# Optimization experiments

Measured on AMD Instinct MI355X. Metric: run time of the kernel, lower is better.

Reference implementation:

```python
import jax, jax.numpy as jnp
import numpy as np
import math

D_DT, D_STATE, D_CONV = 32, 16, 4
C, P, DM, DI = 16, 256, 512, 1024


def setup_inputs() -> dict:
    key = jax.random.key(0)
    ks = jax.random.split(key, 8)
    rn = lambda k, s, sc: jax.random.normal(k, s, jnp.float32) * sc
    # dt bias init as in the module
    u = jax.random.uniform(ks[6], (DI,), jnp.float32)
    dt_bias = jnp.clip(jnp.exp(u * (math.log(0.1) - math.log(0.001))), 0.001, None)
    inv_dt_bias = dt_bias + jnp.log(-jnp.expm1(-dt_bias))
    A_log = jnp.log(jnp.tile(jnp.arange(1, D_STATE + 1, dtype=jnp.float32)[None, :], (DI, 1)))
    return {
        "x": jax.random.normal(ks[0], (C, P, DM), jnp.float32),
        "ssm_state": jnp.zeros((C, DI, D_STATE), jnp.float32),
        "in_w": rn(ks[1], (2 * DI, DM), DM ** -0.5),
        "in_b": jnp.zeros((2 * DI,), jnp.float32),
        "conv_w": rn(ks[2], (DI, DI, D_CONV), (DI * D_CONV) ** -0.5),
        "conv_b": jnp.zeros((DI,), jnp.float32),
        "param_w": rn(ks[3], (D_DT + 2 * D_STATE, DI), DI ** -0.5),
        "param_b": jnp.zeros((D_DT + 2 * D_STATE,), jnp.float32),
        "dt_w": jax.random.uniform(ks[4], (DI, D_DT), jnp.float32, -D_DT ** -0.5, D_DT ** -0.5),
        "dt_b": inv_dt_bias,
        "out_w": rn(ks[5], (DM, DI), DI ** -0.5),
        "out_b": jnp.zeros((DM,), jnp.float32),
        "A_log": A_log,
        "D": jnp.ones((DI,), jnp.float32),
    }


def reference(x, ssm_state, in_w, in_b, conv_w, conv_b, param_w, param_b,
              dt_w, dt_b, out_w, out_b, A_log, D):
    # input projection -> x, z branches          [C,P,2*DI]
    xz = x @ in_w.T + in_b
    xi, z = jnp.split(xz, 2, axis=-1)            # each [C,P,DI]
    # 'same'-ish edge padding along patch axis, then full Conv1d (valid)
    pad = ((0, 0), (D_CONV // 2, (D_CONV + 1) // 2 - 1), (0, 0))
    xi = jnp.pad(xi, pad, mode='edge')
    xi = jnp.swapaxes(xi, -1, -2)                # [C,DI,P+D_CONV-1]
    xi = jax.lax.conv_general_dilated(xi, conv_w, (1,), 'VALID',
                                      dimension_numbers=('NCH', 'OIH', 'NCH'))
    xi = xi + conv_b[None, :, None]
    xi = jax.nn.gelu(jnp.swapaxes(xi, -1, -2))   # [C,P,DI]
    # selective params
    x_db = xi @ param_w.T + param_b              # [C,P,D_DT+2*D_STATE]
    dt, B, Cm = jnp.split(x_db, (D_DT, D_DT + D_STATE), axis=-1)
    dt = jax.nn.softplus(dt @ dt_w.T + dt_b)     # [C,P,DI]
    A = -jnp.exp(A_log)                          # [DI,D_STATE]
    dA = jnp.exp(jnp.einsum('cpd,dn->pcdn', dt, A))   # [P,C,DI,D_STATE]
    dB = jnp.einsum('cpd,cpn->pcdn', dt, B)            # [P,C,DI,D_STATE]
    z = jax.nn.gelu(z)                           # (gelu applied again inside step, as in source)
    Cm_t = jnp.swapaxes(Cm, 0, 1)                # [P,C,D_STATE]
    xi_t = jnp.swapaxes(xi, 0, 1)                # [P,C,DI]
    z_t = jnp.swapaxes(z, 0, 1)                  # [P,C,DI]

    def step(s, data):
        xt, zt, dAt, dBt, Ct = data
        s = s * dAt + xt[..., None] * dBt        # [C,DI,D_STATE]
        y = jnp.einsum('cdn,cn->cd', s, Ct) + D * xt
        return s, y * jax.nn.gelu(zt)            # double gelu: faithful to source

    ssm_state, y = jax.lax.scan(step, ssm_state, (xi_t, z_t, dA, dB, Cm_t))
    y = y @ out_w.T + out_b                      # [P,C,DM]
    return jnp.swapaxes(y, 0, 1), ssm_state
```

## Files before the change

### kernel.cpp

```cpp
#include <hip/hip_runtime.h>
#include <hip/hip_bf16.h>

typedef __hip_bfloat16 bf16;
typedef short bf16x8 __attribute__((ext_vector_type(8)));
typedef float f32x4 __attribute__((ext_vector_type(4)));

#define CC 16
#define PP 256
#define DMH 512
#define DIH 1024
#define MM (CC*PP)
#define NST 16
#define NDT 32
#define LOG2E 1.44269504088896f

__device__ __forceinline__ float b2f(bf16 v){ return __bfloat162float(v); }
__device__ __forceinline__ bf16  f2b(float v){ return __float2bfloat16(v); }
__device__ __forceinline__ float us2f(ushort u){ bf16 h; *(ushort*)&h = u; return __bfloat162float(h); }

__device__ __forceinline__ float geluf(float x){
  const float u = x*(0.7978845608028654f + 0.035677408136300125f*x*x);
  const float e = __builtin_amdgcn_exp2f(2.885390081777927f*u);
  const float t = 1.0f - 2.0f*__builtin_amdgcn_rcpf(e + 1.0f);
  return 0.5f*x*(1.0f + t);
}
__device__ __forceinline__ float softplusf(float x){
  if (x > 20.0f) return x;
  const float e = __builtin_amdgcn_exp2f(x * LOG2E);
  return 0.6931471805599453f * __builtin_amdgcn_logf(1.0f + e);
}

__device__ __forceinline__ void g2l16(const bf16* g, bf16* l){
  __builtin_amdgcn_global_load_lds(
      (const __attribute__((address_space(1))) void*)g,
      (__attribute__((address_space(3))) void*)(uint32_t)(uintptr_t)l,
      16, 0, 0);
}

__global__ void prep_all(const float* __restrict__ x, const float* __restrict__ in_w,
                         const float* __restrict__ out_w, const float* __restrict__ param_w,
                         const float* __restrict__ conv_w, const float* __restrict__ dt_w,
                         const float* __restrict__ in_b, const float* __restrict__ conv_b,
                         float* __restrict__ cb2p,
                         bf16* __restrict__ xbf, bf16* __restrict__ inwz,
                         bf16* __restrict__ outwb, bf16* __restrict__ pwb,
                         bf16* __restrict__ cwT, bf16* __restrict__ inwT,
                         bf16* __restrict__ dtwb)
{
  const int b = blockIdx.x, tid = threadIdx.x;
  if (b < 3136){
    const float* src; bf16* dst; int i;
    if (b < 2048)      { src = x;                       dst = xbf;   i = b*256 + tid; }
    else if (b < 2560) { src = in_w + (size_t)DIH*DMH;  dst = inwz;  i = (b-2048)*256 + tid; }
    else if (b < 3072) { src = out_w;                   dst = outwb; i = (b-2560)*256 + tid; }
    else               { src = param_w;                 dst = pwb;   i = (b-3072)*256 + tid; }
    float4 v = ((const float4*)src)[i];
    bf16 o[4] = {f2b(v.x), f2b(v.y), f2b(v.z), f2b(v.w)};
    *(ushort4*)&dst[(size_t)i*4] = *(const ushort4*)o;
  } else if (b < 7232){
    const size_t idx = (size_t)(b-3136)*256 + tid;
    const float4 v = *(const float4*)(conv_w + idx*4);
    cwT[idx]                     = f2b(v.x);
    cwT[(size_t)DIH*DIH   + idx] = f2b(v.y);
    cwT[(size_t)2*DIH*DIH + idx] = f2b(v.z);
    cwT[(size_t)3*DIH*DIH + idx] = f2b(v.w);
    __shared__ float ls[4];
    const int i = (int)(idx & 1023);
    float acc = (v.x + v.y + v.z + v.w) * in_b[i];
    for (int off = 32; off; off >>= 1) acc += __shfl_down(acc, off);
    if ((tid & 63) == 0) ls[tid >> 6] = acc;
    __syncthreads();
    if (tid == 0){
      const int o   = (int)(idx >> 10);
      const int sub = (b - 3136) & 3;
      float tot = ls[0] + ls[1] + ls[2] + ls[3];
      if (sub == 0) tot += conv_b[o];
      cb2p[sub*DIH + o] = tot;
    }
  } else if (b < 7360){
    __shared__ float T[64][65];
    const int b2 = b - 7232;
    const int i0 = (b2 >> 3)*64, m0 = (b2 & 7)*64;
    const int r = tid >> 2, c0 = (tid & 3)*16;
    #pragma unroll
    for (int t = 0; t < 4; t++){
      float4 v = *(const float4*)&in_w[(size_t)(i0 + r)*DMH + m0 + c0 + t*4];
      T[r][c0+t*4+0] = v.x; T[r][c0+t*4+1] = v.y;
      T[r][c0+t*4+2] = v.z; T[r][c0+t*4+3] = v.w;
    }
    __syncthreads();
    bf16 o[16];
    #pragma unroll
    for (int t = 0; t < 16; t++) o[t] = f2b(T[c0 + t][r]);
    *(ushort4*)&inwT[(size_t)(m0 + r)*DIH + i0 + c0]      = *(const ushort4*)&o[0];
    *(ushort4*)&inwT[(size_t)(m0 + r)*DIH + i0 + c0 + 4]  = *(const ushort4*)&o[4];
    *(ushort4*)&inwT[(size_t)(m0 + r)*DIH + i0 + c0 + 8]  = *(const ushort4*)&o[8];
    *(ushort4*)&inwT[(size_t)(m0 + r)*DIH + i0 + c0 + 12] = *(const ushort4*)&o[12];
  } else {
    const int idx4 = (b-7360)*256 + tid;
    const int d = idx4 >> 4, k4 = (idx4 & 15)*4;
    bf16 o[4] = {};
    if (k4 < 32){
      const float4 v = *(const float4*)&dt_w[(size_t)d*NDT + k4];
      o[0]=f2b(v.x); o[1]=f2b(v.y); o[2]=f2b(v.z); o[3]=f2b(v.w);
    }
    *(ushort4*)&dtwb[(size_t)d*64 + k4] = *(const ushort4*)o;
  }
}

#define TBK 64

template<int EPI, int NFRAG>
__launch_bounds__(256)
__global__ void mfma_gemm(const bf16* __restrict__ A, int lda,
                          const bf16* __restrict__ B, int ldb,
                          const float* __restrict__ bias,
                          float* __restrict__ outF,
                          bf16* __restrict__ outB0,
                          int ldo, int K, int azs, int ozs, int kzs)
{
  __shared__ bf16 As[128*TBK];
  __shared__ bf16 Bs[32*NFRAG*TBK];
  const int tid  = threadIdx.x;
  const int lane = tid & 63;
  const int wave = tid >> 6;
  const int wr = (wave >> 1) * 64;
  const int wc = (wave & 1) * 16 * NFRAG;
  const int mBase = blockIdx.x * 128;
  const int nBase = blockIdx.y * (32*NFRAG);
  A += (size_t)blockIdx.z * azs;
  const int nOff = blockIdx.z * ozs;
  const int koff = blockIdx.z * kzs;

  f32x4 acc[4][NFRAG] = {};

  for (int k0 = 0; k0 < K; k0 += TBK) {
    __syncthreads();
    #pragma unroll
    for (int it = 0; it < 4; it++) {
      const int idx = it*256 + tid;
      const int r = idx >> 3;
      const int cs = (idx & 7) ^ (r & 7);
      const bf16* ga = A + (size_t)(mBase + r)*lda + koff + k0 + cs*8;
      g2l16(ga, &As[(size_t)idx*8]);
    }
    #pragma unroll
    for (int it = 0; it < NFRAG; it++) {
      const int idx = it*256 + tid;
      const int r = idx >> 3;
      const int cs = (idx & 7) ^ (r & 7);
      const bf16* gb = B + (size_t)(nBase + r)*ldb + koff + k0 + cs*8;
      g2l16(gb, &Bs[(size_t)idx*8]);
    }
    __syncthreads();
    #pragma unroll
    for (int ks = 0; ks < 2; ks++) {
      bf16x8 af[4], bfr[NFRAG];
      #pragma unroll
      for (int r = 0; r < 4; r++){
        const int rr = wr + r*16 + (lane & 15);
        const int ch = (ks*4 + (lane>>4)) ^ (rr & 7);
        af[r] = *(const bf16x8*)&As[rr*TBK + ch*8];
      }
      #pragma unroll
      for (int c = 0; c < NFRAG; c++){
        const int rn = wc + c*16 + (lane & 15);
        const int ch = (ks*4 + (lane>>4)) ^ (rn & 7);
        bfr[c] = *(const bf16x8*)&Bs[rn*TBK + ch*8];
      }
      #pragma unroll
      for (int r = 0; r < 4; r++)
        #pragma unroll
        for (int c = 0; c < NFRAG; c++)
          acc[r][c] = __builtin_amdgcn_mfma_f32_16x16x32_bf16(af[r], bfr[c], acc[r][c], 0, 0, 0);
    }
  }

  const int col0 = lane & 15;
  const int row0 = (lane >> 4) * 4;
  #pragma unroll
  for (int r = 0; r < 4; r++) {
    #pragma unroll
    for (int c = 0; c < NFRAG; c++) {
      #pragma unroll
      for (int reg = 0; reg < 4; reg++) {
        const int m = mBase + wr + r*16 + row0 + reg;
        const int n = nBase + wc + c*16 + col0;
        const float av = acc[r][c][reg];
        if (EPI == 0) {
          outF[(size_t)m*ldo + n] = av + bias[n];
        } else if (EPI == 2) {
          outB0[(size_t)m*ldo + n] = f2b(geluf(geluf(av + bias[n])));
        } else if (EPI == 3) {
          outB0[(size_t)m*ldo + n + nOff] = f2b(av);
        } else if (EPI == 5) {
          const float dtv = softplusf(av + bias[n]);
          bf16 dh = f2b(dtv);
          ((ushort*)outB0)[(size_t)m*ldo + n] = *(const ushort*)&dh;
        } else if (EPI == 7) {
          const float vv = av + bias[n];
          if (n < 32) {
            bf16 dh = f2b(vv);
            ((ushort*)outB0)[(size_t)m*64 + n] = *(const ushort*)&dh;
          } else {
            ((ushort*)outB0)[(size_t)m*64 + n] = 0;
            outF[(size_t)m*32 + (n - 32)] = vv;
          }
        }
      }
    }
  }
}

__launch_bounds__(256)
__global__ void mfma_conv(const bf16* __restrict__ A,
                          const bf16* __restrict__ B,
                          const float* __restrict__ bias,
                          bf16* __restrict__ outB)
{
  __shared__ bf16 As[132*64];
  __shared__ bf16 Bs[128*64];
  const int tid = threadIdx.x;
  const int lane = tid & 63;
  const int wave = tid >> 6;
  const int wr = (wave >> 1) * 64;
  const int wc = (wave & 1) * 16;
  const int mBase = blockIdx.x * 128;
  const int nBase = blockIdx.y * 32;
  const int cc = mBase >> 8;
  const int q  = mBase & 255;

  f32x4 acc[4][4] = {};

  for (int k0 = 0; k0 < DMH; k0 += 64) {
    __syncthreads();
    #pragma unroll
    for (int it = 0; it < 5; it++) {
      const int idx = it*256 + tid;
      if (it < 4 || idx < 1056) {
        const int h = idx >> 3;
        const int cs = (idx & 7) ^ (h & 7);
        int p = q - 2 + h;
        p = min(max(p, 0), PP-1);
        g2l16(A + ((size_t)(cc*PP + p))*DMH + k0 + cs*8, &As[(size_t)idx*8]);
      }
    }
    #pragma unroll
    for (int it = 0; it < 4; it++) {
      const int idx = it*256 + tid;
      const int r = idx >> 3;
      const int tap = r >> 5, o = r & 31;
      const int cs = (idx & 7) ^ (r & 7);
      g2l16(B + (size_t)(nBase + o)*(4*DMH) + tap*DMH + k0 + cs*8, &Bs[(size_t)idx*8]);
    }
    __syncthreads();
    #pragma unroll
    for (int ks = 0; ks < 2; ks++) {
      #pragma unroll
      for (int t = 0; t < 4; t++) {
        bf16x8 bft;
        {
          const int rn = t*32 + wc + (lane & 15);
          const int ch = (ks*4 + (lane>>4)) ^ (rn & 7);
          bft = *(const bf16x8*)&Bs[rn*64 + ch*8];
        }
        #pragma unroll
        for (int r = 0; r < 4; r++) {
          const int h = wr + r*16 + (lane & 15) + t;
          const int ch = (ks*4 + (lane>>4)) ^ (h & 7);
          bf16x8 af = *(const bf16x8*)&As[h*64 + ch*8];
          acc[r][t] = __builtin_amdgcn_mfma_f32_16x16x32_bf16(af, bft, acc[r][t], 0, 0, 0);
        }
      }
    }
  }
  const int col0 = lane & 15;
  const int row0 = (lane >> 4) * 4;
  const int nn = nBase + wc + col0;
  const float bv = bias[nn] + bias[DIH + nn] + bias[2*DIH + nn] + bias[3*DIH + nn];
  #pragma unroll
  for (int r = 0; r < 4; r++) {
    #pragma unroll
    for (int reg = 0; reg < 4; reg++) {
      const int m = mBase + wr + r*16 + row0 + reg;
      const float av = acc[r][0][reg] + acc[r][1][reg] + acc[r][2][reg] + acc[r][3][reg];
      outB[(size_t)m*DIH + nn] = f2b(geluf(av + bv));
    }
  }
}

__launch_bounds__(256, 2)
__global__ void scan_v6(const float* __restrict__ bcg, const bf16* __restrict__ xi,
                        const bf16* __restrict__ gz, const bf16* __restrict__ dtp,
                        const float* __restrict__ A_log, const float* __restrict__ Dp,
                        const float* __restrict__ s0,
                        bf16* __restrict__ ypre, float* __restrict__ state_out)
{
  const int dg = blockIdx.x;
  const int tid = threadIdx.x;
  const int u = tid >> 7, ut = tid & 127;
  const int c = blockIdx.y*2 + u;
  const int dl = ut >> 3, ng = ut & 7;
  const int d0 = dg*16;
  const int d  = d0 + dl;
  const int base_m = c*PP;

  __shared__ float  bcT[2][3][32][20];
  __shared__ ushort dtT[2][3][16][24];
  __shared__ ushort xiT[2][3][16][24];
  __shared__ ushort gzT[2][3][16][24];
  __shared__ float  ybF[2][2][16][17];
  __shared__ ushort outT[2][16][24];
  __shared__ float  DvT[2][16];

  if (ut < 16) DvT[u][ut] = Dp[d0 + ut];
  const float2 al = *(const float2*)&A_log[(size_t)d*NST + 2*ng];
  const float a20 = -__expf(al.x)*LOG2E;
  const float a21 = -__expf(al.y)*LOG2E;
  float2 s = *(const float2*)&s0[((size_t)c*DIH + d)*NST + 2*ng];

  const int br = ut >> 3, bc4 = (ut & 7)*4;
  float4 bc_r; uint4 sec_r;

#define STAGE_LOAD(mm) do { \
    bc_r = *(const float4*)&bcg[(size_t)((mm) + br)*32 + bc4]; \
    if (ut < 32)      sec_r = *(const uint4*)&((const ushort*)dtp)[(size_t)((mm) + (ut>>1))*DIH + d0 + (ut&1)*8]; \
    else if (ut < 64) sec_r = *(const uint4*)&((const ushort*)xi)[(size_t)((mm) + ((ut-32)>>1))*DIH + d0 + ((ut-32)&1)*8]; \
    else if (ut < 96) sec_r = *(const uint4*)&((const ushort*)gz)[(size_t)((mm) + ((ut-64)>>1))*DIH + d0 + ((ut-64)&1)*8]; \
  } while(0)
#define STAGE_COMMIT(nbuf) do { \
    bcT[u][nbuf][bc4+0][br] = bc_r.x; \
    bcT[u][nbuf][bc4+1][br] = bc_r.y; \
    bcT[u][nbuf][bc4+2][br] = bc_r.z; \
    bcT[u][nbuf][bc4+3][br] = bc_r.w; \
    if (ut < 32){ \
      const int jj = ut >> 1, hh = (ut & 1)*8; \
      _Pragma("unroll") \
      for (int t = 0; t < 8; t++) dtT[u][nbuf][hh+t][jj] = ((const ushort*)&sec_r)[t]; \
    } else if (ut < 64){ \
      const int jj = (ut-32) >> 1, hh = ((ut-32) & 1)*8; \
      _Pragma("unroll") \
      for (int t = 0; t < 8; t++) xiT[u][nbuf][hh+t][jj] = ((const ushort*)&sec_r)[t]; \
    } else if (ut < 96){ \
      *(uint4*)&gzT[u][nbuf][(ut-64)>>1][((ut-64)&1)*8] = sec_r; \
    } \
  } while(0)

  STAGE_LOAD(base_m);
  STAGE_COMMIT(0);
  __syncthreads();

  for (int g = 0; g < 16; ++g){
    const int buf = g % 3, nb = (g+1) % 3, yb = g & 1;
    const int m0 = base_m + g*16;
    if (g < 15) STAGE_LOAD(m0 + 16);
    uint4 dtv4[2], xiv4[2];
    dtv4[0] = *(const uint4*)&dtT[u][buf][dl][0];
    dtv4[1] = *(const uint4*)&dtT[u][buf][dl][8];
    xiv4[0] = *(const uint4*)&xiT[u][buf][dl][0];
    xiv4[1] = *(const uint4*)&xiT[u][buf][dl][8];
    float4 Bv0[4], Bv1[4], Cv0[4], Cv1[4];
    #pragma unroll
    for (int cc = 0; cc < 4; cc++){
      Bv0[cc] = *(const float4*)&bcT[u][buf][2*ng    ][cc*4];
      Bv1[cc] = *(const float4*)&bcT[u][buf][2*ng+1  ][cc*4];
      Cv0[cc] = *(const float4*)&bcT[u][buf][16+2*ng ][cc*4];
      Cv1[cc] = *(const float4*)&bcT[u][buf][17+2*ng ][cc*4];
    }
    float e0[16], e1[16], t0[16], t1[16];
    #pragma unroll
    for (int j = 0; j < 16; j++){
      const float dtv = us2f(((const ushort*)dtv4)[j]);
      const float xiv = us2f(((const ushort*)xiv4)[j]);
      const float dtxi = dtv * xiv;
      e0[j] = __builtin_amdgcn_exp2f(dtv*a20);
      e1[j] = __builtin_amdgcn_exp2f(dtv*a21);
      t0[j] = dtxi * ((const float*)Bv0)[j];
      t1[j] = dtxi * ((const float*)Bv1)[j];
    }
    #pragma unroll
    for (int j = 0; j < 16; j++){
      s.x = fmaf(s.x, e0[j], t0[j]);
      s.y = fmaf(s.y, e1[j], t1[j]);
      float y = fmaf(s.y, ((const float*)Cv1)[j], s.x*((const float*)Cv0)[j]);
      int t;
      t = __builtin_amdgcn_update_dpp(0, __float_as_int(y), 0x111, 0xf, 0xf, true);
      y += __int_as_float(t);
      t = __builtin_amdgcn_update_dpp(0, __float_as_int(y), 0x112, 0xf, 0xf, true);
      y += __int_as_float(t);
      t = __builtin_amdgcn_update_dpp(0, __float_as_int(y), 0x114, 0xf, 0xf, true);
      y += __int_as_float(t);
      if (ng == 7) ybF[u][yb][j][dl] = y;
    }
    if (g < 15) STAGE_COMMIT(nb);
    __syncthreads();
    {
      const int ej = ut >> 3, eg = ut & 7;
      #pragma unroll
      for (int q = 0; q < 2; q++){
        const int ed = 2*eg + q;
        bf16 hv = f2b((ybF[u][yb][ej][ed] + DvT[u][ed]*us2f(xiT[u][buf][ed][ej]))
                      * us2f(gzT[u][buf][ej][ed]));
        outT[u][ej][ed] = *(const ushort*)&hv;
      }
      if (eg < 2)
        *(uint4*)((ushort*)ypre + (size_t)(m0+ej)*DIH + d0 + eg*8) = *(const uint4*)&outT[u][ej][eg*8];
    }
  }
  *(float2*)&state_out[((size_t)c*DIH + d)*NST + 2*ng] = s;
#undef STAGE_LOAD
#undef STAGE_COMMIT
}

extern "C" void kernel_launch(void* const* d_in, const int* in_sizes, int n_in,
                              void* d_out, int out_size, void* d_ws, size_t ws_size,
                              hipStream_t stream) {
  const float* x       = (const float*)d_in[0];
  const float* s0      = (const float*)d_in[1];
  const float* in_w    = (const float*)d_in[2];
  const float* in_b    = (const float*)d_in[3];
  const float* conv_w  = (const float*)d_in[4];
  const float* conv_b  = (const float*)d_in[5];
  const float* param_w = (const float*)d_in[6];
  const float* param_b = (const float*)d_in[7];
  const float* dt_w    = (const float*)d_in[8];
  const float* dt_b    = (const float*)d_in[9];
  const float* out_w   = (const float*)d_in[10];
  const float* out_b   = (const float*)d_in[11];
  const float* A_log   = (const float*)d_in[12];
  const float* Dp      = (const float*)d_in[13];

  char* ws = (char*)d_ws;
  bf16*   xi    = (bf16*)ws;   ws += (size_t)MM*DIH*2;
  bf16*   gz    = (bf16*)ws;   ws += (size_t)MM*DIH*2;
  float*  bcg   = (float*)ws;  ws += (size_t)MM*32*4;
  bf16*   xdbb  = (bf16*)ws;   ws += (size_t)MM*64*2;
  float*  cb2p  = (float*)ws;  ws += 4*DIH*4;
  bf16*   ypre  = (bf16*)ws;   ws += (size_t)MM*DIH*2;
  bf16*   outwb = (bf16*)ws;   ws += (size_t)DMH*DIH*2;
  bf16*   pwb   = (bf16*)ws;   ws += (size_t)64*DIH*2;
  bf16*   dtwb  = (bf16*)ws;   ws += (size_t)DIH*64*2;
  char*   U     = ws;          ws += (size_t)32*1024*1024;
  bf16* Wfb  = (bf16*)(U);
  bf16* xbf  = (bf16*)(U + (size_t) 4*1024*1024);
  bf16* inwz = (bf16*)(U + (size_t) 8*1024*1024);
  bf16* inwT = (bf16*)(U + (size_t) 9*1024*1024);
  bf16* cwT  = (bf16*)(U + (size_t)10*1024*1024);
  bf16*  dtp = (bf16*)(U + (size_t)16*1024*1024);

  float* y_out  = (float*)d_out;
  float* st_out = y_out + (size_t)MM*DMH;

  prep_all<<<7424, 256, 0, stream>>>(x, in_w, out_w, param_w, conv_w, dt_w,
                                     in_b, conv_b, cb2p,
                                     xbf, inwz, outwb, pwb, cwT, inwT, dtwb);

  mfma_gemm<3,1><<<dim3(DIH/128, DMH/32, 4), 256, 0, stream>>>(
      cwT, DIH, inwT, DIH, nullptr, nullptr, Wfb, 4*DMH, DIH, DIH*DIH, DMH, 0);
  mfma_gemm<2,1><<<dim3(MM/128, DIH/32), 256, 0, stream>>>(
      xbf, DMH, inwz, DMH, in_b + DIH, nullptr, gz, DIH, DMH, 0, 0, 0);
  mfma_conv<<<dim3(MM/128, DIH/32), 256, 0, stream>>>(xbf, Wfb, cb2p, xi);
  mfma_gemm<7,1><<<dim3(MM/128, 2), 256, 0, stream>>>(
      xi, DIH, pwb, DIH, param_b, bcg, (bf16*)xdbb, 64, DIH, 0, 0, 0);
  mfma_gemm<5,1><<<dim3(MM/128, DIH/32), 256, 0, stream>>>(
      xdbb, 64, dtwb, 64, dt_b, nullptr, (bf16*)dtp, DIH, 64, 0, 0, 0);
  scan_v6<<<dim3(64, CC/2), 256, 0, stream>>>(bcg, xi, gz, dtp, A_log, Dp,
                                              s0, ypre, st_out);
  mfma_gemm<0,1><<<dim3(MM/128, DMH/32), 256, 0, stream>>>(
      ypre, DIH, outwb, DIH, out_b, y_out, nullptr, DMH, DIH, 0, 0, 0);
}
```

Baseline: 213.8 us.

## Split selective scan in time halves with a mid-state pre-pass kernel

Adds a lightweight scan_mid kernel that runs the state recurrence over the first 128 patches only, skipping the C projection and output, and stores the intermediate state. The main scan kernel then runs each chunk as two independent 128-step halves in parallel: the first starts from the initial state, the second from the stored mid state. This halves the serial dependency length of the output-producing scan and doubles its grid size. In exchange the first half of the recurrence is computed twice and an extra launch plus mid-state round trip through memory is added.

Measured after the change: 225.4 us. 5.4% more time.

```diff
diff --git a/kernel.cpp b/kernel.cpp
--- a/kernel.cpp
+++ b/kernel.cpp
@@ -290,11 +290,9 @@
 }
 
 __launch_bounds__(256, 2)
-__global__ void scan_v6(const float* __restrict__ bcg, const bf16* __restrict__ xi,
-                        const bf16* __restrict__ gz, const bf16* __restrict__ dtp,
-                        const float* __restrict__ A_log, const float* __restrict__ Dp,
-                        const float* __restrict__ s0,
-                        bf16* __restrict__ ypre, float* __restrict__ state_out)
+__global__ void scan_mid(const float* __restrict__ bcg, const bf16* __restrict__ xi,
+                         const bf16* __restrict__ dtp, const float* __restrict__ A_log,
+                         const float* __restrict__ s0, float* __restrict__ sMid)
 {
   const int dg = blockIdx.x;
   const int tid = threadIdx.x;
@@ -305,6 +303,88 @@
   const int d  = d0 + dl;
   const int base_m = c*PP;
 
+  __shared__ float  bT[2][3][16][20];
+  __shared__ ushort dtT[2][3][16][24];
+  __shared__ ushort xiT[2][3][16][24];
+
+  const float2 al = *(const float2*)&A_log[(size_t)d*NST + 2*ng];
+  const float a20 = -__expf(al.x)*LOG2E;
+  const float a21 = -__expf(al.y)*LOG2E;
+  float2 s = *(const float2*)&s0[((size_t)c*DIH + d)*NST + 2*ng];
+
+  float4 b_r; uint4 sec_r;
+
+#define MLOAD(mm) do { \
+    if (ut < 64)      b_r  = *(const float4*)&bcg[(size_t)((mm) + (ut>>2))*32 + (ut&3)*4]; \
+    else if (ut < 96) sec_r = *(const uint4*)&((const ushort*)dtp)[(size_t)((mm) + ((ut-64)>>1))*DIH + d0 + ((ut-64)&1)*8]; \
+    else              sec_r = *(const uint4*)&((const ushort*)xi)[(size_t)((mm) + ((ut-96)>>1))*DIH + d0 + ((ut-96)&1)*8]; \
+  } while(0)
+#define MCOMMIT(nbuf) do { \
+    if (ut < 64){ \
+      const int rr = ut>>2, q4 = (ut&3)*4; \
+      bT[u][nbuf][q4+0][rr] = b_r.x; bT[u][nbuf][q4+1][rr] = b_r.y; \
+      bT[u][nbuf][q4+2][rr] = b_r.z; bT[u][nbuf][q4+3][rr] = b_r.w; \
+    } else if (ut < 96){ \
+      const int jj = (ut-64)>>1, hh = ((ut-64)&1)*8; \
+      _Pragma("unroll") \
+      for (int t = 0; t < 8; t++) dtT[u][nbuf][hh+t][jj] = ((const ushort*)&sec_r)[t]; \
+    } else { \
+      const int jj = (ut-96)>>1, hh = ((ut-96)&1)*8; \
+      _Pragma("unroll") \
+      for (int t = 0; t < 8; t++) xiT[u][nbuf][hh+t][jj] = ((const ushort*)&sec_r)[t]; \
+    } \
+  } while(0)
+
+  MLOAD(base_m);
+  MCOMMIT(0);
+  __syncthreads();
+
+  for (int g = 0; g < 8; ++g){
+    const int buf = g % 3, nb = (g+1) % 3;
+    if (g < 7) MLOAD(base_m + (g+1)*16);
+    uint4 dtv4[2], xiv4[2];
+    dtv4[0] = *(const uint4*)&dtT[u][buf][dl][0];
+    dtv4[1] = *(const uint4*)&dtT[u][buf][dl][8];
+    xiv4[0] = *(const uint4*)&xiT[u][buf][dl][0];
+    xiv4[1] = *(const uint4*)&xiT[u][buf][dl][8];
+    float4 Bv0[4], Bv1[4];
+    #pragma unroll
+    for (int q4 = 0; q4 < 4; q4++){
+      Bv0[q4] = *(const float4*)&bT[u][buf][2*ng  ][q4*4];
+      Bv1[q4] = *(const float4*)&bT[u][buf][2*ng+1][q4*4];
+    }
+    #pragma unroll
+    for (int j = 0; j < 16; j++){
+      const float dtv = us2f(((const ushort*)dtv4)[j]);
+      const float xiv = us2f(((const ushort*)xiv4)[j]);
+      const float dtxi = dtv * xiv;
+      s.x = fmaf(s.x, __builtin_amdgcn_exp2f(dtv*a20), dtxi*((const float*)Bv0)[j]);
+      s.y = fmaf(s.y, __builtin_amdgcn_exp2f(dtv*a21), dtxi*((const float*)Bv1)[j]);
+    }
+    if (g < 7) MCOMMIT(nb);
+    __syncthreads();
+  }
+  *(float2*)&sMid[((size_t)c*DIH + d)*NST + 2*ng] = s;
+#undef MLOAD
+#undef MCOMMIT
+}
+
+__launch_bounds__(256, 2)
+__global__ void scan_v7(const float* __restrict__ bcg, const bf16* __restrict__ xi,
+                        const bf16* __restrict__ gz, const bf16* __restrict__ dtp,
+                        const float* __restrict__ A_log, const float* __restrict__ Dp,
+                        const float* __restrict__ s0, const float* __restrict__ sMid,
+                        bf16* __restrict__ ypre, float* __restrict__ state_out)
+{
+  const int dg = blockIdx.x;
+  const int tid = threadIdx.x;
+  const int u = tid >> 7, ut = tid & 127;
+  const int c = blockIdx.y;
+  const int dl = ut >> 3, ng = ut & 7;
+  const int d0 = dg*16;
+  const int d  = d0 + dl;
+  const int base_m = c*PP + u*128;
+
   __shared__ float  bcT[2][3][32][20];
   __shared__ ushort dtT[2][3][16][24];
   __shared__ ushort xiT[2][3][16][24];
@@ -317,7 +397,8 @@
   const float2 al = *(const float2*)&A_log[(size_t)d*NST + 2*ng];
   const float a20 = -__expf(al.x)*LOG2E;
   const float a21 = -__expf(al.y)*LOG2E;
-  float2 s = *(const float2*)&s0[((size_t)c*DIH + d)*NST + 2*ng];
+  const float* sini = u ? sMid : s0;
+  float2 s = *(const float2*)&sini[((size_t)c*DIH + d)*NST + 2*ng];
 
   const int br = ut >> 3, bc4 = (ut & 7)*4;
   float4 bc_r; uint4 sec_r;
@@ -350,10 +431,10 @@
   STAGE_COMMIT(0);
   __syncthreads();
 
-  for (int g = 0; g < 16; ++g){
+  for (int g = 0; g < 8; ++g){
     const int buf = g % 3, nb = (g+1) % 3, yb = g & 1;
     const int m0 = base_m + g*16;
-    if (g < 15) STAGE_LOAD(m0 + 16);
+    if (g < 7) STAGE_LOAD(m0 + 16);
     uint4 dtv4[2], xiv4[2];
     dtv4[0] = *(const uint4*)&dtT[u][buf][dl][0];
     dtv4[1] = *(const uint4*)&dtT[u][buf][dl][8];
@@ -361,11 +442,11 @@
     xiv4[1] = *(const uint4*)&xiT[u][buf][dl][8];
     float4 Bv0[4], Bv1[4], Cv0[4], Cv1[4];
     #pragma unroll
-    for (int cc = 0; cc < 4; cc++){
-      Bv0[cc] = *(const float4*)&bcT[u][buf][2*ng    ][cc*4];
-      Bv1[cc] = *(const float4*)&bcT[u][buf][2*ng+1  ][cc*4];
-      Cv0[cc] = *(const float4*)&bcT[u][buf][16+2*ng ][cc*4];
-      Cv1[cc] = *(const float4*)&bcT[u][buf][17+2*ng ][cc*4];
+    for (int q4 = 0; q4 < 4; q4++){
+      Bv0[q4] = *(const float4*)&bcT[u][buf][2*ng    ][q4*4];
+      Bv1[q4] = *(const float4*)&bcT[u][buf][2*ng+1  ][q4*4];
+      Cv0[q4] = *(const float4*)&bcT[u][buf][16+2*ng ][q4*4];
+      Cv1[q4] = *(const float4*)&bcT[u][buf][17+2*ng ][q4*4];
     }
     float e0[16], e1[16], t0[16], t1[16];
     #pragma unroll
@@ -392,7 +473,7 @@
       y += __int_as_float(t);
       if (ng == 7) ybF[u][yb][j][dl] = y;
     }
-    if (g < 15) STAGE_COMMIT(nb);
+    if (g < 7) STAGE_COMMIT(nb);
     __syncthreads();
     {
       const int ej = ut >> 3, eg = ut & 7;
@@ -407,7 +488,8 @@
         *(uint4*)((ushort*)ypre + (size_t)(m0+ej)*DIH + d0 + eg*8) = *(const uint4*)&outT[u][ej][eg*8];
     }
   }
-  *(float2*)&state_out[((size_t)c*DIH + d)*NST + 2*ng] = s;
+  if (u == 1)
+    *(float2*)&state_out[((size_t)c*DIH + d)*NST + 2*ng] = s;
 #undef STAGE_LOAD
 #undef STAGE_COMMIT
 }
@@ -446,7 +528,8 @@
   bf16* inwz = (bf16*)(U + (size_t) 8*1024*1024);
   bf16* inwT = (bf16*)(U + (size_t) 9*1024*1024);
   bf16* cwT  = (bf16*)(U + (size_t)10*1024*1024);
-  bf16*  dtp = (bf16*)(U + (size_t)16*1024*1024);
+  bf16*  dtp  = (bf16*)(U + (size_t)16*1024*1024);
+  float* sMid = (float*)(U + (size_t)24*1024*1024);
 
   float* y_out  = (float*)d_out;
   float* st_out = y_out + (size_t)MM*DMH;
@@ -464,8 +547,9 @@
       xi, DIH, pwb, DIH, param_b, bcg, (bf16*)xdbb, 64, DIH, 0, 0, 0);
   mfma_gemm<5,1><<<dim3(MM/128, DIH/32), 256, 0, stream>>>(
       xdbb, 64, dtwb, 64, dt_b, nullptr, (bf16*)dtp, DIH, 64, 0, 0, 0);
-  scan_v6<<<dim3(64, CC/2), 256, 0, stream>>>(bcg, xi, gz, dtp, A_log, Dp,
-                                              s0, ypre, st_out);
+  scan_mid<<<dim3(64, CC/2), 256, 0, stream>>>(bcg, xi, dtp, A_log, s0, sMid);
+  scan_v7<<<dim3(64, CC), 256, 0, stream>>>(bcg, xi, gz, dtp, A_log, Dp,
+                                            s0, sMid, ypre, st_out);
   mfma_gemm<0,1><<<dim3(MM/128, DMH/32), 256, 0, stream>>>(
       ypre, DIH, outwb, DIH, out_b, y_out, nullptr, DMH, DIH, 0, 0, 0);
 }
```
